# Performance work log

Hardware: AMD Instinct MI355X
Metric: run time of the kernel (lower is better)

The kernel has to match this reference:

```python
import math
import jax, jax.numpy as jnp
import numpy as np

D_MODEL = 896
N_HEADS = 14
D_HEAD = D_MODEL // N_HEADS  # 64
ROPE_BASE = 10000.0
LN_EPS = 1e-5
B, N = 8, 1024


def setup_inputs() -> dict:
    key = jax.random.key(0)
    ks = jax.random.split(key, 12)
    s = 1.0 / math.sqrt(D_MODEL)
    return {
        "node_features": jax.random.normal(ks[0], (B, N, D_MODEL), jnp.float32),
        "adj": jax.random.uniform(ks[1], (N, N), jnp.float32),
        "wind_dirs": jax.random.uniform(ks[2], (B, N), jnp.float32),
        "bearings": jax.random.uniform(ks[3], (N, N), jnp.float32),
        "Wq": jax.random.normal(ks[4], (D_MODEL, D_MODEL), jnp.float32) * s,
        "Wk": jax.random.normal(ks[5], (D_MODEL, D_MODEL), jnp.float32) * s,
        "Wv": jax.random.normal(ks[6], (D_MODEL, D_MODEL), jnp.float32) * s,
        "Wo": jax.random.normal(ks[7], (D_MODEL, D_MODEL), jnp.float32) * s,
        "ln_g": jnp.ones((D_MODEL,), jnp.float32),
        "ln_b": jnp.zeros((D_MODEL,), jnp.float32),
        "wind_w": jax.random.normal(ks[8], (2, N_HEADS), jnp.float32) * (1.0 / math.sqrt(2.0)),
        "wind_b": jnp.zeros((N_HEADS,), jnp.float32),
    }


def _layernorm(x, g, b):
    mu = jnp.mean(x, axis=-1, keepdims=True)
    var = jnp.var(x, axis=-1, keepdims=True)
    return (x - mu) * jax.lax.rsqrt(var + LN_EPS) * g + b


def _apply_rotary(x, cos_h, sin_h):
    # x: (B,H,N,d_head); cos_h/sin_h: (N, d_head//2)
    d_half = x.shape[-1] // 2
    x1, x2 = x[..., :d_half], x[..., d_half:]
    return jnp.concatenate([x1 * cos_h - x2 * sin_h, x2 * cos_h + x1 * sin_h], axis=-1)


def reference(node_features, adj, wind_dirs, bearings, Wq, Wk, Wv, Wo, ln_g, ln_b, wind_w, wind_b):
    Bb, Nn, D = node_features.shape
    residual = node_features
    x = _layernorm(node_features, ln_g, ln_b)

    def proj(W):
        return (x @ W).reshape(Bb, Nn, N_HEADS, D_HEAD).transpose(0, 2, 1, 3)  # (B,H,N,dh)

    Q, K, V = proj(Wq), proj(Wk), proj(Wv)

    # RoPE: cos/sin halves (first d_half entries of the duplicated freq table)
    inv_freq = 1.0 / (ROPE_BASE ** (jnp.arange(0, D_HEAD, 2, dtype=jnp.float32) / D_HEAD))
    freqs = jnp.arange(Nn, dtype=jnp.float32)[:, None] * inv_freq[None, :]  # (N, dh/2)
    cos_h, sin_h = jnp.cos(freqs), jnp.sin(freqs)
    Q = _apply_rotary(Q, cos_h, sin_h)
    K = _apply_rotary(K, cos_h, sin_h)

    attn = jnp.einsum("bhqd,bhkd->bhqk", Q, K) / math.sqrt(D_HEAD)
    adj_mask = (adj > 0)[None, None, :, :]
    attn = jnp.where(adj_mask, attn, -1e30)

    # wind-direction dynamic edge bias
    reverse_bearings = (bearings.T + 180.0) % 360.0  # (N,N)
    alignment = jnp.cos(jnp.deg2rad(wind_dirs[:, :, None] - reverse_bearings[None]))  # (B,N,N)
    dist_feat = jnp.broadcast_to(adj[None], (Bb, Nn, Nn))
    edge_features = jnp.stack([alignment, dist_feat], axis=-1)  # (B,N,N,2)
    wind_bias = jnp.tanh(edge_features @ wind_w + wind_b)  # (B,N,N,H)
    attn = attn + wind_bias.transpose(0, 3, 1, 2)  # (B,H,N,N)

    attn = jax.nn.softmax(attn, axis=-1)  # dropout is identity in eval
    out = jnp.einsum("bhqk,bhkd->bhqd", attn, V)
    out = out.transpose(0, 2, 1, 3).reshape(Bb, Nn, D) @ Wo
    return residual + out
```

## Files before the change

kernel.cpp:

```cpp
#include <hip/hip_runtime.h>
#include <hip/hip_bf16.h>
#include <math.h>

#define B_ 8
#define N_ 1024
#define H_ 14
#define DH_ 64
#define D_ 896
#define M_ (B_*N_)
#define DQKV_ 2688

#define TWO_LOG2E_ 2.8853900817779268f
#define BIAS_C_   (-15.869645449778597f)
#define QSCALE_     0.18033688011112043f

typedef __attribute__((ext_vector_type(8))) short bf16x8;
typedef __attribute__((ext_vector_type(4))) short bf16x4;
typedef __attribute__((ext_vector_type(4))) float f32x4;
typedef __attribute__((ext_vector_type(4))) unsigned u32x4;

__device__ __forceinline__ float bf2f(short s){
  unsigned u = ((unsigned)(unsigned short)s) << 16;
  union { unsigned u; float f; } c; c.u = u; return c.f;
}
__device__ __forceinline__ short f2bf(float f){
  union { float f; unsigned u; } c; c.f = f;
  unsigned u = c.u;
  unsigned r = (u + 0x7FFFu + ((u >> 16) & 1u)) >> 16;
  return (short)(unsigned short)r;
}
__device__ __forceinline__ float asf(unsigned u){
  union { unsigned u; float f; } c; c.u = u; return c.f;
}

__global__ __launch_bounds__(256) void ln_kernel(const float* __restrict__ x,
                                                 const float* __restrict__ g,
                                                 const float* __restrict__ bb,
                                                 short* __restrict__ y)
{
  int row = blockIdx.x;
  const float* xr = x + (size_t)row * D_;
  float s = 0.f, s2 = 0.f;
  for (int i = threadIdx.x; i < D_; i += 256){
    float v = xr[i]; s += v; s2 = fmaf(v, v, s2);
  }
  #pragma unroll
  for (int off = 32; off > 0; off >>= 1){
    s  += __shfl_down(s,  off, 64);
    s2 += __shfl_down(s2, off, 64);
  }
  __shared__ float rs_[4], rs2_[4];
  int wv = threadIdx.x >> 6;
  if ((threadIdx.x & 63) == 0){ rs_[wv] = s; rs2_[wv] = s2; }
  __syncthreads();
  float ts  = rs_[0] + rs_[1] + rs_[2] + rs_[3];
  float ts2 = rs2_[0] + rs2_[1] + rs2_[2] + rs2_[3];
  float mu  = ts * (1.f / D_);
  float var = ts2 * (1.f / D_) - mu * mu;
  float rstd = rsqrtf(var + 1e-5f);
  short* yr = y + (size_t)row * D_;
  for (int i = threadIdx.x; i < D_; i += 256){
    yr[i] = f2bf((xr[i] - mu) * rstd * g[i] + bb[i]);
  }
}

__global__ __launch_bounds__(256) void transpose_kernel(
    const float* __restrict__ Wq, const float* __restrict__ Wk,
    const float* __restrict__ Wv, const float* __restrict__ Wo,
    short* __restrict__ WqkvT, short* __restrict__ WoT)
{
  __shared__ short t[64][72];
  int z = blockIdx.z;
  const float* W = (z == 0) ? Wq : (z == 1) ? Wk : (z == 2) ? Wv : Wo;
  int kb = blockIdx.x * 64, nb = blockIdx.y * 64;
  int c0 = (threadIdx.x & 7) * 8;
  int r0 = threadIdx.x >> 3;
  #pragma unroll
  for (int rr = 0; rr < 64; rr += 32){
    const float* src = &W[(size_t)(kb + r0 + rr) * D_ + nb + c0];
    float4 a = *(const float4*)src;
    float4 b = *(const float4*)(src + 4);
    short* dstl = &t[r0 + rr][c0];
    dstl[0] = f2bf(a.x); dstl[1] = f2bf(a.y); dstl[2] = f2bf(a.z); dstl[3] = f2bf(a.w);
    dstl[4] = f2bf(b.x); dstl[5] = f2bf(b.y); dstl[6] = f2bf(b.z); dstl[7] = f2bf(b.w);
  }
  __syncthreads();
  short* dst = (z < 3) ? (WqkvT + (size_t)(z * D_) * D_) : WoT;
  #pragma unroll
  for (int rr = 0; rr < 64; rr += 32){
    int n = nb + r0 + rr;
    bf16x8 v;
    #pragma unroll
    for (int j = 0; j < 8; j++) v[j] = t[c0 + j][r0 + rr];
    *(bf16x8*)&dst[(size_t)n * D_ + kb + c0] = v;
  }
}

__global__ __launch_bounds__(256) void prep_kernel(
    const float* __restrict__ adj, const float* __restrict__ brg,
    unsigned* __restrict__ csb, short* __restrict__ adjT)
{
  int kt = blockIdx.x, qt = blockIdx.y;
  int r  = threadIdx.x >> 2;
  int c0 = (threadIdx.x & 3) * 16;
  {
    int k = kt * 64 + r;
    const float* bp = brg + (size_t)k * N_ + qt * 64 + c0;
    unsigned* cp = csb + (size_t)k * N_ + qt * 64 + c0;
    #pragma unroll
    for (int i = 0; i < 16; i += 4){
      float4 bv = *(const float4*)(bp + i);
      float b4[4] = { bv.x, bv.y, bv.z, bv.w };
      unsigned o[4];
      #pragma unroll
      for (int j = 0; j < 4; j++){
        float Br = (b4[j] + 180.f) * 0.017453292519943295f;
        float sB, cB;
        __sincosf(Br, &sB, &cB);
        o[j] = ((unsigned)(unsigned short)f2bf(cB)) |
               (((unsigned)(unsigned short)f2bf(sB)) << 16);
      }
      *(uint4*)(cp + i) = make_uint4(o[0], o[1], o[2], o[3]);
    }
  }
  __shared__ short tt[64][72];
  {
    int q = qt * 64 + r;
    const float* ap = adj + (size_t)q * N_ + kt * 64 + c0;
    #pragma unroll
    for (int i = 0; i < 16; i += 4){
      float4 av = *(const float4*)(ap + i);
      tt[r][c0 + i]     = f2bf(av.x);
      tt[r][c0 + i + 1] = f2bf(av.y);
      tt[r][c0 + i + 2] = f2bf(av.z);
      tt[r][c0 + i + 3] = f2bf(av.w);
    }
  }
  __syncthreads();
  {
    int k = kt * 64 + r;
    short* op = adjT + (size_t)k * N_ + qt * 64 + c0;
    bf16x8 v0, v1;
    #pragma unroll
    for (int j = 0; j < 8; j++){ v0[j] = tt[c0 + j][r]; v1[j] = tt[c0 + 8 + j][r]; }
    *(bf16x8*)op = v0;
    *(bf16x8*)(op + 8) = v1;
  }
}

__global__ __launch_bounds__(256) void align_kernel(const float* __restrict__ brg,
                                                    const float* __restrict__ wdir,
                                                    short* __restrict__ alignT)
{
  int kt = blockIdx.x;
  int b  = blockIdx.y;
  __shared__ float cA[N_], sA[N_];
  for (int q = threadIdx.x; q < N_; q += 256){
    float A = wdir[(size_t)b * N_ + q] * 0.017453292519943295f;
    float s, c; __sincosf(A, &s, &c);
    sA[q] = s; cA[q] = c;
  }
  __syncthreads();
  int q4 = threadIdx.x * 4;
  for (int kr = 0; kr < 64; kr++){
    int k = kt * 64 + kr;
    float4 bv = *(const float4*)(brg + (size_t)k * N_ + q4);
    float b4[4] = { bv.x, bv.y, bv.z, bv.w };
    unsigned oo[2];
    #pragma unroll
    for (int p = 0; p < 2; p++){
      unsigned lo = 0, hi = 0;
      #pragma unroll
      for (int j = 0; j < 2; j++){
        int qq = q4 + p * 2 + j;
        float Br = (b4[p * 2 + j] + 180.f) * 0.017453292519943295f;
        float sB, cB; __sincosf(Br, &sB, &cB);
        float al = fmaf(cA[qq], cB, sA[qq] * sB);
        unsigned v = (unsigned)(unsigned short)f2bf(al);
        if (j == 0) lo = v; else hi = v;
      }
      oo[p] = lo | (hi << 16);
    }
    *(uint2*)(alignT + ((size_t)b * N_ + k) * N_ + q4) = make_uint2(oo[0], oo[1]);
  }
}

__global__ __launch_bounds__(256) void gemm_bt(const short* __restrict__ A,
                                               const short* __restrict__ Bt,
                                               short* __restrict__ C,
                                               float* __restrict__ Cf,
                                               const float* __restrict__ residf,
                                               int N, int rope)
{
  const int K = D_;
  __shared__ short As[128 * 32];
  __shared__ short Bs[128 * 32];
  int tid  = threadIdx.x;
  int wave = tid >> 6;
  int lane = tid & 63;
  int quad = lane >> 4;
  int l16  = lane & 15;
  int wr = wave >> 1, wc = wave & 1;
  int m0 = blockIdx.x * 128;
  int n0 = blockIdx.y * 128;

  f32x4 acc[4][4];
  #pragma unroll
  for (int i = 0; i < 4; i++)
    #pragma unroll
    for (int j = 0; j < 4; j++)
      acc[i][j] = (f32x4){0.f, 0.f, 0.f, 0.f};

  for (int k0 = 0; k0 < K; k0 += 32){
    __syncthreads();
    #pragma unroll
    for (int it = 0; it < 2; ++it){
      int c   = tid + it * 256;
      int row = c >> 2;
      int cc  = c & 3;
      const short* ga = A  + (size_t)(m0 + row) * K + k0 + cc * 8;
      const short* gb = Bt + (size_t)(n0 + row) * K + k0 + cc * 8;
      short* la = As + (size_t)(wave * 64 + it * 256) * 8;
      short* lb = Bs + (size_t)(wave * 64 + it * 256) * 8;
      __builtin_amdgcn_global_load_lds((const __attribute__((address_space(1))) void*)ga,
                                       (__attribute__((address_space(3))) void*)la, 16, 0, 0);
      __builtin_amdgcn_global_load_lds((const __attribute__((address_space(1))) void*)gb,
                                       (__attribute__((address_space(3))) void*)lb, 16, 0, 0);
    }
    __syncthreads();

    bf16x8 af[4], bfr[4];
    #pragma unroll
    for (int i = 0; i < 4; i++)
      af[i] = *(const bf16x8*)(As + (size_t)(wr * 64 + i * 16 + l16) * 32 + quad * 8);
    #pragma unroll
    for (int j = 0; j < 4; j++)
      bfr[j] = *(const bf16x8*)(Bs + (size_t)(wc * 64 + j * 16 + l16) * 32 + quad * 8);
    #pragma unroll
    for (int i = 0; i < 4; i++)
      #pragma unroll
      for (int j = 0; j < 4; j++)
        acc[i][j] = __builtin_amdgcn_mfma_f32_16x16x32_bf16(af[i], bfr[j], acc[i][j], 0, 0, 0);
  }

  if (rope){
    int cb  = n0 + wc * 64;
    int mat = cb / D_;
    if (mat < 2){
      float scale = (mat == 0) ? QSCALE_ : 1.0f;
      float invf0 = exp2f(-0.4152410118609203f * (float)l16);
      float invf1 = invf0 * 0.01f;
      #pragma unroll
      for (int i = 0; i < 4; i++){
        #pragma unroll
        for (int rr = 0; rr < 4; rr++){
          int r = m0 + wr * 64 + i * 16 + quad * 4 + rr;
          float nseq = (float)(r & (N_ - 1));
          float s0, c0v, s1, c1v;
          __sincosf(nseq * invf0, &s0, &c0v);
          __sincosf(nseq * invf1, &s1, &c1v);
          float x1 = acc[i][0][rr], x2 = acc[i][2][rr];
          acc[i][0][rr] = (x1 * c0v - x2 * s0) * scale;
          acc[i][2][rr] = (x2 * c0v + x1 * s0) * scale;
          x1 = acc[i][1][rr]; x2 = acc[i][3][rr];
          acc[i][1][rr] = (x1 * c1v - x2 * s1) * scale;
          acc[i][3][rr] = (x2 * c1v + x1 * s1) * scale;
        }
      }
    }
  }

  #pragma unroll
  for (int i = 0; i < 4; i++){
    #pragma unroll
    for (int rr = 0; rr < 4; rr++){
      int r = m0 + wr * 64 + i * 16 + quad * 4 + rr;
      size_t rowoff = (size_t)r * N;
      #pragma unroll
      for (int j = 0; j < 4; j++){
        int cidx = n0 + wc * 64 + j * 16 + l16;
        float v = acc[i][j][rr];
        if (Cf){
          Cf[rowoff + cidx] = v + residf[rowoff + cidx];
        } else {
          C[rowoff + cidx] = f2bf(v);
        }
      }
    }
  }
}

__global__ __launch_bounds__(512, 4)
__global__ void attn_dummy();

template<int PRE>
__global__ __launch_bounds__(512, 4) void attn_kernel(
    const short* __restrict__ QKV,
    const unsigned* __restrict__ csb,
    const short* __restrict__ adjT,
    const short* __restrict__ alignT,
    const float* __restrict__ wind_dirs,
    const float* __restrict__ wind_w,
    const float* __restrict__ wind_b,
    short* __restrict__ outb)
{
  __shared__ short K_s[64 * 72];
  __shared__ short V_t[64 * 76];
  __shared__ short P_s[128 * 76];

  int bid = blockIdx.x;
  int qt  = bid & 7;
  int hh  = (bid >> 3) % H_;
  int b   = bid / (8 * H_);
  int q0  = qt * 128;

  int t    = threadIdx.x;
  int w    = t >> 6;
  int lane = t & 63;
  int quad = lane >> 4;
  int l16  = lane & 15;

  const short* qp = QKV + ((size_t)(b * N_) + q0 + w * 16 + l16) * DQKV_ + hh * DH_;
  bf16x8 qf0 = *(const bf16x8*)(qp + quad * 8);
  bf16x8 qf1 = *(const bf16x8*)(qp + 32 + quad * 8);

  float cA[4], sA[4];
  if (!PRE){
    #pragma unroll
    for (int rr = 0; rr < 4; rr++){
      float wd = wind_dirs[(size_t)b * N_ + q0 + w * 16 + quad * 4 + rr];
      float A  = wd * 0.017453292519943295f;
      sA[rr] = __sinf(A);
      cA[rr] = __cosf(A);
    }
  }
  float w0m = wind_w[hh]      * TWO_LOG2E_;
  float w1m = wind_w[H_ + hh] * TWO_LOG2E_;
  float wbm = wind_b[hh]      * TWO_LOG2E_;

  float l[4] = {0.f, 0.f, 0.f, 0.f};
  f32x4 O[4];
  #pragma unroll
  for (int dc = 0; dc < 4; dc++) O[dc] = (f32x4){0.f, 0.f, 0.f, 0.f};

  int kr  = t >> 3, kc8 = (t & 7) * 8;
  int vk2 = (t >> 4) * 2, vd4 = (t & 15) * 4;
  const short* kg0 = QKV + ((size_t)(b * N_) + kr)  * DQKV_ + D_     + hh * DH_ + kc8;
  const short* vg0 = QKV + ((size_t)(b * N_) + vk2) * DQKV_ + 2 * D_ + hh * DH_ + vd4;

  bf16x8 pk  = *(const bf16x8*)kg0;
  bf16x4 pv0 = *(const bf16x4*)vg0;
  bf16x4 pv1 = *(const bf16x4*)(vg0 + DQKV_);

  for (int kt = 0; kt < 16; ++kt){
    int k0 = kt * 64;
    __syncthreads();
    *(bf16x8*)(K_s + kr * 72 + kc8) = pk;
    #pragma unroll
    for (int j = 0; j < 4; j++){
      unsigned pv = ((unsigned)(unsigned short)pv0[j]) |
                    (((unsigned)(unsigned short)pv1[j]) << 16);
      *(unsigned*)(V_t + (vd4 + j) * 76 + vk2) = pv;
    }
    __syncthreads();

    {
      int kn = (kt < 15) ? (k0 + 64) : k0;
      pk  = *(const bf16x8*)(kg0 + (size_t)kn * DQKV_);
      pv0 = *(const bf16x4*)(vg0 + (size_t)kn * DQKV_);
      pv1 = *(const bf16x4*)(vg0 + (size_t)(kn + 1) * DQKV_);
    }

    u32x4 cs4a[4]; bf16x4 al4a[4]; bf16x4 av4a[4];
    #pragma unroll
    for (int jc = 0; jc < 4; jc++){
      size_t off = (size_t)(k0 + jc * 16 + l16) * N_ + q0 + w * 16 + quad * 4;
      if (PRE) al4a[jc] = *(const bf16x4*)(alignT + (size_t)b * N_ * N_ + off);
      else     cs4a[jc] = *(const u32x4*)(csb + off);
      av4a[jc] = *(const bf16x4*)(adjT + off);
    }

    f32x4 S[4];
    __builtin_amdgcn_s_setprio(1);
    #pragma unroll
    for (int jc = 0; jc < 4; jc++){
      S[jc] = (f32x4){0.f, 0.f, 0.f, 0.f};
      bf16x8 kf0 = *(const bf16x8*)(K_s + (jc * 16 + l16) * 72 + quad * 8);
      bf16x8 kf1 = *(const bf16x8*)(K_s + (jc * 16 + l16) * 72 + 32 + quad * 8);
      S[jc] = __builtin_amdgcn_mfma_f32_16x16x32_bf16(qf0, kf0, S[jc], 0, 0, 0);
      S[jc] = __builtin_amdgcn_mfma_f32_16x16x32_bf16(qf1, kf1, S[jc], 0, 0, 0);
    }
    __builtin_amdgcn_s_setprio(0);

    #pragma unroll
    for (int jc = 0; jc < 4; jc++){
      #pragma unroll
      for (int rr = 0; rr < 4; rr++){
        float av = bf2f(av4a[jc][rr]);
        float align;
        if (PRE){
          align = bf2f(al4a[jc][rr]);
        } else {
          unsigned u = cs4a[jc][rr];
          float cB = asf(u << 16);
          float sB = asf(u & 0xffff0000u);
          align = cA[rr] * cB + sA[rr] * sB;
        }
        float z2 = fmaf(align, w0m, fmaf(av, w1m, wbm));
        float e2 = __builtin_amdgcn_exp2f(z2);
        float rc = __builtin_amdgcn_rcpf(e2 + 1.f);
        float bias2 = fmaf(-TWO_LOG2E_, rc, BIAS_C_);
        float sv = (av > 0.f ? S[jc][rr] : -1e30f) + bias2;
        float e = __builtin_amdgcn_exp2f(sv);
        l[rr] += e;
        P_s[(w * 16 + quad * 4 + rr) * 76 + jc * 16 + l16] = f2bf(e);
      }
    }

    __builtin_amdgcn_s_setprio(1);
    #pragma unroll
    for (int kc = 0; kc < 2; kc++){
      const short* pp = P_s + (w * 16 + l16) * 76 + kc * 32 + quad * 8;
      bf16x4 p0 = *(const bf16x4*)pp;
      bf16x4 p1 = *(const bf16x4*)(pp + 4);
      bf16x8 pf = { p0[0], p0[1], p0[2], p0[3], p1[0], p1[1], p1[2], p1[3] };
      #pragma unroll
      for (int dc = 0; dc < 4; dc++){
        const short* vp = V_t + (dc * 16 + l16) * 76 + kc * 32 + quad * 8;
        bf16x4 u0 = *(const bf16x4*)vp;
        bf16x4 u1 = *(const bf16x4*)(vp + 4);
        bf16x8 vf = { u0[0], u0[1], u0[2], u0[3], u1[0], u1[1], u1[2], u1[3] };
        O[dc] = __builtin_amdgcn_mfma_f32_16x16x32_bf16(pf, vf, O[dc], 0, 0, 0);
      }
    }
    __builtin_amdgcn_s_setprio(0);
  }

  float rl[4];
  #pragma unroll
  for (int rr = 0; rr < 4; rr++){
    float rs = l[rr];
    rs += __shfl_xor(rs, 1);
    rs += __shfl_xor(rs, 2);
    rs += __shfl_xor(rs, 4);
    rs += __shfl_xor(rs, 8);
    rl[rr] = 1.f / rs;
  }
  short* op = outb + ((size_t)(b * N_) + q0 + w * 16) * D_ + hh * DH_;
  #pragma unroll
  for (int rr = 0; rr < 4; rr++)
    #pragma unroll
    for (int dc = 0; dc < 4; dc++)
      op[(size_t)(quad * 4 + rr) * D_ + dc * 16 + l16] = f2bf(O[dc][rr] * rl[rr]);
}

extern "C" void kernel_launch(void* const* d_in, const int* in_sizes, int n_in,
                              void* d_out, int out_size, void* d_ws, size_t ws_size,
                              hipStream_t stream)
{
  const float* nf   = (const float*)d_in[0];
  const float* adj  = (const float*)d_in[1];
  const float* wdir = (const float*)d_in[2];
  const float* brg  = (const float*)d_in[3];
  const float* Wq   = (const float*)d_in[4];
  const float* Wk   = (const float*)d_in[5];
  const float* Wv   = (const float*)d_in[6];
  const float* Wo   = (const float*)d_in[7];
  const float* lng  = (const float*)d_in[8];
  const float* lnb  = (const float*)d_in[9];
  const float* ww   = (const float*)d_in[10];
  const float* wbb  = (const float*)d_in[11];
  float* out = (float*)d_out;

  short* base = (short*)d_ws;
  size_t sh = 0;
  short* xln   = base + sh;  sh += (size_t)M_ * D_;
  short* WqkvT = base + sh;  sh += (size_t)DQKV_ * D_;
  short* WoT   = base + sh;  sh += (size_t)D_ * D_;
  short* QKV   = base + sh;  sh += (size_t)M_ * DQKV_;
  unsigned* csb = (unsigned*)(base + sh); sh += (size_t)N_ * N_ * 2;
  short* adjT  = base + sh;  sh += (size_t)N_ * N_;
  short* alignT = base + sh; sh += (size_t)B_ * N_ * N_;
  size_t need_pre = sh * sizeof(short);
  bool pre = (ws_size >= need_pre);

  ln_kernel<<<M_, 256, 0, stream>>>(nf, lng, lnb, xln);
  transpose_kernel<<<dim3(14, 14, 4), 256, 0, stream>>>(Wq, Wk, Wv, Wo, WqkvT, WoT);
  prep_kernel<<<dim3(16, 16), 256, 0, stream>>>(adj, brg, csb, adjT);
  if (pre)
    align_kernel<<<dim3(16, 8), 256, 0, stream>>>(brg, wdir, alignT);
  gemm_bt<<<dim3(M_ / 128, DQKV_ / 128), 256, 0, stream>>>(xln, WqkvT, QKV, nullptr, nullptr, DQKV_, 1);
  if (pre)
    attn_kernel<1><<<B_ * H_ * 8, 512, 0, stream>>>(QKV, csb, adjT, alignT, wdir, ww, wbb, xln);
  else
    attn_kernel<0><<<B_ * H_ * 8, 512, 0, stream>>>(QKV, csb, adjT, alignT, wdir, ww, wbb, xln);
  gemm_bt<<<dim3(M_ / 128, D_ / 128), 256, 0, stream>>>(xln, WoT, nullptr, out, nf, D_, 0);
}
```

Before: 405.7 us.

## Fuse alignment precompute into prep kernel and prefetch bias tiles in attention

Removes the separate align_kernel and computes the per-batch alignment table inside prep_kernel, reusing the bearing sin/cos already computed there so each is evaluated once instead of once per batch, with better parallelism (256 blocks instead of 128). In the attention kernel, the bias/adjacency loads for the next key tile are issued after the softmax step, so their latency overlaps the PV MFMAs rather than stalling before the next iteration. The __syncthreads calls are replaced by an LDS-only waitcnt plus barrier so outstanding global prefetches need not drain at each barrier. The prefetch costs extra registers in a kernel bounded at 512 threads with 4 blocks per CU, and the last iteration reloads a tile it never uses.

```diff
diff --git a/kernel.cpp b/kernel.cpp
--- a/kernel.cpp
+++ b/kernel.cpp
@@ -32,6 +32,9 @@
 __device__ __forceinline__ float asf(unsigned u){
   union { unsigned u; float f; } c; c.u = u; return c.f;
 }
+
+#define BAR_LDS() do { asm volatile("s_waitcnt lgkmcnt(0)" ::: "memory"); \
+                       __builtin_amdgcn_s_barrier(); } while (0)
 
 __global__ __launch_bounds__(256) void ln_kernel(const float* __restrict__ x,
                                                  const float* __restrict__ g,
@@ -98,32 +101,26 @@
 
 __global__ __launch_bounds__(256) void prep_kernel(
     const float* __restrict__ adj, const float* __restrict__ brg,
-    unsigned* __restrict__ csb, short* __restrict__ adjT)
+    const float* __restrict__ wdir,
+    unsigned* __restrict__ csb, short* __restrict__ adjT,
+    short* __restrict__ alignT, int do_align)
 {
   int kt = blockIdx.x, qt = blockIdx.y;
+  __shared__ short tt[64][72];
+  __shared__ float cA_[8][64], sA_[8][64];
+
+  if (do_align){
+    for (int idx = threadIdx.x; idx < 8 * 64; idx += 256){
+      int b = idx >> 6, q = idx & 63;
+      float A = wdir[(size_t)b * N_ + qt * 64 + q] * 0.017453292519943295f;
+      float s, c; __sincosf(A, &s, &c);
+      sA_[b][q] = s; cA_[b][q] = c;
+    }
+  }
+
   int r  = threadIdx.x >> 2;
   int c0 = (threadIdx.x & 3) * 16;
-  {
-    int k = kt * 64 + r;
-    const float* bp = brg + (size_t)k * N_ + qt * 64 + c0;
-    unsigned* cp = csb + (size_t)k * N_ + qt * 64 + c0;
-    #pragma unroll
-    for (int i = 0; i < 16; i += 4){
-      float4 bv = *(const float4*)(bp + i);
-      float b4[4] = { bv.x, bv.y, bv.z, bv.w };
-      unsigned o[4];
-      #pragma unroll
-      for (int j = 0; j < 4; j++){
-        float Br = (b4[j] + 180.f) * 0.017453292519943295f;
-        float sB, cB;
-        __sincosf(Br, &sB, &cB);
-        o[j] = ((unsigned)(unsigned short)f2bf(cB)) |
-               (((unsigned)(unsigned short)f2bf(sB)) << 16);
-      }
-      *(uint4*)(cp + i) = make_uint4(o[0], o[1], o[2], o[3]);
-    }
-  }
-  __shared__ short tt[64][72];
+
   {
     int q = qt * 64 + r;
     const float* ap = adj + (size_t)q * N_ + kt * 64 + c0;
@@ -137,6 +134,48 @@
     }
   }
   __syncthreads();
+
+  {
+    int k = kt * 64 + r;
+    const float* bp = brg + (size_t)k * N_ + qt * 64 + c0;
+    unsigned* cp = csb + (size_t)k * N_ + qt * 64 + c0;
+    #pragma unroll
+    for (int i = 0; i < 16; i += 4){
+      float4 bv = *(const float4*)(bp + i);
+      float b4[4] = { bv.x, bv.y, bv.z, bv.w };
+      float cB[4], sB[4];
+      unsigned o[4];
+      #pragma unroll
+      for (int j = 0; j < 4; j++){
+        float Br = (b4[j] + 180.f) * 0.017453292519943295f;
+        __sincosf(Br, &sB[j], &cB[j]);
+        o[j] = ((unsigned)(unsigned short)f2bf(cB[j])) |
+               (((unsigned)(unsigned short)f2bf(sB[j])) << 16);
+      }
+      *(uint4*)(cp + i) = make_uint4(o[0], o[1], o[2], o[3]);
+      if (do_align){
+        #pragma unroll
+        for (int b = 0; b < 8; b++){
+          unsigned w2[2];
+          #pragma unroll
+          for (int p = 0; p < 2; p++){
+            unsigned lo = 0, hi = 0;
+            #pragma unroll
+            for (int j = 0; j < 2; j++){
+              int q = c0 + i + p * 2 + j;
+              float al = fmaf(cA_[b][q], cB[p * 2 + j], sA_[b][q] * sB[p * 2 + j]);
+              unsigned v = (unsigned)(unsigned short)f2bf(al);
+              if (j == 0) lo = v; else hi = v;
+            }
+            w2[p] = lo | (hi << 16);
+          }
+          *(uint2*)(alignT + ((size_t)b * N_ + k) * N_ + qt * 64 + c0 + i) =
+              make_uint2(w2[0], w2[1]);
+        }
+      }
+    }
+  }
+
   {
     int k = kt * 64 + r;
     short* op = adjT + (size_t)k * N_ + qt * 64 + c0;
@@ -145,43 +184,6 @@
     for (int j = 0; j < 8; j++){ v0[j] = tt[c0 + j][r]; v1[j] = tt[c0 + 8 + j][r]; }
     *(bf16x8*)op = v0;
     *(bf16x8*)(op + 8) = v1;
-  }
-}
-
-__global__ __launch_bounds__(256) void align_kernel(const float* __restrict__ brg,
-                                                    const float* __restrict__ wdir,
-                                                    short* __restrict__ alignT)
-{
-  int kt = blockIdx.x;
-  int b  = blockIdx.y;
-  __shared__ float cA[N_], sA[N_];
-  for (int q = threadIdx.x; q < N_; q += 256){
-    float A = wdir[(size_t)b * N_ + q] * 0.017453292519943295f;
-    float s, c; __sincosf(A, &s, &c);
-    sA[q] = s; cA[q] = c;
-  }
-  __syncthreads();
-  int q4 = threadIdx.x * 4;
-  for (int kr = 0; kr < 64; kr++){
-    int k = kt * 64 + kr;
-    float4 bv = *(const float4*)(brg + (size_t)k * N_ + q4);
-    float b4[4] = { bv.x, bv.y, bv.z, bv.w };
-    unsigned oo[2];
-    #pragma unroll
-    for (int p = 0; p < 2; p++){
-      unsigned lo = 0, hi = 0;
-      #pragma unroll
-      for (int j = 0; j < 2; j++){
-        int qq = q4 + p * 2 + j;
-        float Br = (b4[p * 2 + j] + 180.f) * 0.017453292519943295f;
-        float sB, cB; __sincosf(Br, &sB, &cB);
-        float al = fmaf(cA[qq], cB, sA[qq] * sB);
-        unsigned v = (unsigned)(unsigned short)f2bf(al);
-        if (j == 0) lo = v; else hi = v;
-      }
-      oo[p] = lo | (hi << 16);
-    }
-    *(uint2*)(alignT + ((size_t)b * N_ + k) * N_ + q4) = make_uint2(oo[0], oo[1]);
   }
 }
 
@@ -290,9 +292,6 @@
   }
 }
 
-__global__ __launch_bounds__(512, 4)
-__global__ void attn_dummy();
-
 template<int PRE>
 __global__ __launch_bounds__(512, 4) void attn_kernel(
     const short* __restrict__ QKV,
@@ -352,9 +351,19 @@
   bf16x4 pv0 = *(const bf16x4*)vg0;
   bf16x4 pv1 = *(const bf16x4*)(vg0 + DQKV_);
 
+  size_t bias_q = (size_t)(q0 + w * 16 + quad * 4);
+  u32x4 cs4a[4]; bf16x4 al4a[4]; bf16x4 av4a[4];
+  #pragma unroll
+  for (int jc = 0; jc < 4; jc++){
+    size_t off = (size_t)(jc * 16 + l16) * N_ + bias_q;
+    if (PRE) al4a[jc] = *(const bf16x4*)(alignT + (size_t)b * N_ * N_ + off);
+    else     cs4a[jc] = *(const u32x4*)(csb + off);
+    av4a[jc] = *(const bf16x4*)(adjT + off);
+  }
+
   for (int kt = 0; kt < 16; ++kt){
     int k0 = kt * 64;
-    __syncthreads();
+    BAR_LDS();
     *(bf16x8*)(K_s + kr * 72 + kc8) = pk;
     #pragma unroll
     for (int j = 0; j < 4; j++){
@@ -362,23 +371,12 @@
                     (((unsigned)(unsigned short)pv1[j]) << 16);
       *(unsigned*)(V_t + (vd4 + j) * 76 + vk2) = pv;
     }
-    __syncthreads();
-
-    {
-      int kn = (kt < 15) ? (k0 + 64) : k0;
-      pk  = *(const bf16x8*)(kg0 + (size_t)kn * DQKV_);
-      pv0 = *(const bf16x4*)(vg0 + (size_t)kn * DQKV_);
-      pv1 = *(const bf16x4*)(vg0 + (size_t)(kn + 1) * DQKV_);
-    }
-
-    u32x4 cs4a[4]; bf16x4 al4a[4]; bf16x4 av4a[4];
-    #pragma unroll
-    for (int jc = 0; jc < 4; jc++){
-      size_t off = (size_t)(k0 + jc * 16 + l16) * N_ + q0 + w * 16 + quad * 4;
-      if (PRE) al4a[jc] = *(const bf16x4*)(alignT + (size_t)b * N_ * N_ + off);
-      else     cs4a[jc] = *(const u32x4*)(csb + off);
-      av4a[jc] = *(const bf16x4*)(adjT + off);
-    }
+    BAR_LDS();
+
+    int kn = (kt < 15) ? (k0 + 64) : k0;
+    pk  = *(const bf16x8*)(kg0 + (size_t)kn * DQKV_);
+    pv0 = *(const bf16x4*)(vg0 + (size_t)kn * DQKV_);
+    pv1 = *(const bf16x4*)(vg0 + (size_t)(kn + 1) * DQKV_);
 
     f32x4 S[4];
     __builtin_amdgcn_s_setprio(1);
@@ -417,6 +415,14 @@
       }
     }
 
+    #pragma unroll
+    for (int jc = 0; jc < 4; jc++){
+      size_t off = (size_t)(kn + jc * 16 + l16) * N_ + bias_q;
+      if (PRE) al4a[jc] = *(const bf16x4*)(alignT + (size_t)b * N_ * N_ + off);
+      else     cs4a[jc] = *(const u32x4*)(csb + off);
+      av4a[jc] = *(const bf16x4*)(adjT + off);
+    }
+
     __builtin_amdgcn_s_setprio(1);
     #pragma unroll
     for (int kc = 0; kc < 2; kc++){
@@ -486,9 +492,7 @@
 
   ln_kernel<<<M_, 256, 0, stream>>>(nf, lng, lnb, xln);
   transpose_kernel<<<dim3(14, 14, 4), 256, 0, stream>>>(Wq, Wk, Wv, Wo, WqkvT, WoT);
-  prep_kernel<<<dim3(16, 16), 256, 0, stream>>>(adj, brg, csb, adjT);
-  if (pre)
-    align_kernel<<<dim3(16, 8), 256, 0, stream>>>(brg, wdir, alignT);
+  prep_kernel<<<dim3(16, 16), 256, 0, stream>>>(adj, brg, wdir, csb, adjT, alignT, pre ? 1 : 0);
   gemm_bt<<<dim3(M_ / 128, DQKV_ / 128), 256, 0, stream>>>(xln, WqkvT, QKV, nullptr, nullptr, DQKV_, 1);
   if (pre)
     attn_kernel<1><<<B_ * H_ * 8, 512, 0, stream>>>(QKV, csb, adjT, alignT, wdir, ww, wbb, xln);
```

Result: faster. 388.9 us (-4.1%).
